# Performance work log

Measured on AMD Instinct MI355X. Metric: run time of the kernel, lower is better.

The kernel has to match this reference:

```python
import jax, jax.numpy as jnp
import numpy as np

DN = ('NCDHW', 'OIDHW', 'NCDHW')

def conv3d(x, w, b=None):
    y = jax.lax.conv_general_dilated(x, w, (1, 1, 1), 'SAME', dimension_numbers=DN)
    if b is not None:
        y = y + b[None, :, None, None, None]
    return y

def adaptive_conv(x, w):
    # x: [N,C,D,H,W], w: [N,27,D,H,W] (L1-normalized over channel dim)
    D, H, W = x.shape[2], x.shape[3], x.shape[4]
    p = jnp.pad(x, ((0, 0), (0, 0), (1, 1), (1, 1), (1, 1)))
    out = jnp.zeros_like(x)
    for i in range(3):
        for j in range(3):
            for k in range(3):
                t = i * 9 + j * 3 + k
                out = out + p[:, :, i:i + D, j:j + H, k:k + W] * w[:, t:t + 1]
    return out

def l1_normalize(w):
    # torch F.normalize(dim=1, p=1): denom clamped to 1e-12
    denom = jnp.maximum(jnp.sum(jnp.abs(w), axis=1, keepdims=True), 1e-12)
    return w / denom

def adaptive_block(x, w1, b1, w2, weights_src=None):
    src = x if weights_src is None else weights_src
    h = jax.nn.relu(conv3d(src, w1, b1))
    w = l1_normalize(conv3d(h, w2))  # [N,27,D,H,W]
    for _ in range(3):
        x = adaptive_conv(x, w)
    return x

def setup_inputs() -> dict:
    key = jax.random.key(0)
    ks = jax.random.split(key, 16)
    s = 0.05
    inp = {
        'x': jax.random.normal(ks[0], (1, 8, 128, 128, 128), dtype=jnp.float32),
        'ac1_w1': jax.random.normal(ks[1], (8, 8, 3, 3, 3), dtype=jnp.float32) * s,
        'ac1_b1': jnp.zeros((8,), dtype=jnp.float32),
        'ac1_w2': jax.random.normal(ks[2], (27, 8, 3, 3, 3), dtype=jnp.float32) * s,
        'ac2_w1': jax.random.normal(ks[3], (8, 8, 3, 3, 3), dtype=jnp.float32) * s,
        'ac2_b1': jnp.zeros((8,), dtype=jnp.float32),
        'ac2_w2': jax.random.normal(ks[4], (27, 8, 3, 3, 3), dtype=jnp.float32) * s,
        'ac3_w1': jax.random.normal(ks[5], (8, 8, 3, 3, 3), dtype=jnp.float32) * s,
        'ac3_b1': jnp.zeros((8,), dtype=jnp.float32),
        'ac3_w2': jax.random.normal(ks[6], (27, 8, 3, 3, 3), dtype=jnp.float32) * s,
        'mid_w': jax.random.normal(ks[7], (8, 8, 3, 3, 3), dtype=jnp.float32) * s,
        'mid_b': jnp.zeros((8,), dtype=jnp.float32),
        'out_w': jax.random.normal(ks[8], (1, 8, 3, 3, 3), dtype=jnp.float32) * s,
        'out_b': jnp.zeros((1,), dtype=jnp.float32),
    }
    return inp

def reference(x, ac1_w1, ac1_b1, ac1_w2, ac2_w1, ac2_b1, ac2_w2,
              ac3_w1, ac3_b1, ac3_w2, mid_w, mid_b, out_w, out_b):
    mid = adaptive_block(x, ac1_w1, ac1_b1, ac1_w2)
    mid = conv3d(mid, mid_w, mid_b)
    mid = adaptive_block(mid, ac2_w1, ac2_b1, ac2_w2)
    final = conv3d(mid, out_w, out_b)  # [N,1,D,H,W]
    final = adaptive_block(final, ac3_w1, ac3_b1, ac3_w2, weights_src=mid)
    return jnp.tanh(final)
```

## Files before the change

### kernel.cpp

```cpp
#include <hip/hip_runtime.h>
#include <math.h>

#define DSZ 128
#define VOX (DSZ*DSZ*DSZ)
#define PD  130

typedef _Float16 half8 __attribute__((ext_vector_type(8)));
typedef _Float16 half4 __attribute__((ext_vector_type(4)));
typedef _Float16 half2v __attribute__((ext_vector_type(2)));
typedef float float4v __attribute__((ext_vector_type(4)));


template<int CH>
__global__ __launch_bounds__(256) void zero_halo(_Float16* __restrict__ P)
{
    const int t = blockIdx.x * 256 + threadIdx.x;
    if (t >= PD * PD) return;
    const int zp = t / PD;
    const int yp = t - zp * PD;
    _Float16* row = P + (size_t)t * PD * CH;
    if (zp == 0 || zp == PD - 1 || yp == 0 || yp == PD - 1) {
        if (CH == 8) {
            half8 zz = {};
            for (int x = 0; x < PD; ++x) *(half8*)&row[x * 8] = zz;
        } else {
            for (int x = 0; x < PD; ++x) row[x] = (_Float16)0.0f;
        }
    } else {
        if (CH == 8) {
            half8 zz = {};
            *(half8*)&row[0] = zz;
            *(half8*)&row[(PD - 1) * 8] = zz;
        } else {
            row[0] = (_Float16)0.0f;
            row[PD - 1] = (_Float16)0.0f;
        }
    }
}

__global__ __launch_bounds__(256) void preformat(const float* __restrict__ w1a, const float* __restrict__ w1b,
                                                 const float* __restrict__ w1c, const float* __restrict__ outw,
                                                 const float* __restrict__ midw,
                                                 const float* __restrict__ w2a, const float* __restrict__ w2b,
                                                 const float* __restrict__ w2c, _Float16* __restrict__ WF)
{
    const int bid = blockIdx.x, tid = threadIdx.x;
    const float* src;
    _Float16* dst;
    int nelem, sz;
    if (bid < 3)       { src = bid == 0 ? w1a : bid == 1 ? w1b : w1c; dst = WF + bid * 3712; nelem = 8 * 216; sz = 16 * 29; }
    else if (bid == 3) { src = outw; dst = WF + 3 * 3712; nelem = 216;     sz = 16 * 29; }
    else if (bid == 4) { src = midw; dst = WF + 4 * 3712; nelem = 8 * 216; sz = 16 * 29; }
    else               { src = bid == 5 ? w2a : bid == 6 ? w2b : w2c; dst = WF + 5 * 3712 + (bid - 5) * 7424; nelem = 27 * 216; sz = 32 * 29; }
    for (int i = tid; i < sz; i += 256) ((half8*)dst)[i] = half8{};
    __syncthreads();
    for (int i = tid; i < nelem; i += 256) {
        const int oc = i / 216;
        const int rem = i - oc * 216;
        const int ic = rem / 27;
        const int tap = rem - ic * 27;
        dst[(oc * 29 + tap) * 8 + ic] = (_Float16)src[i];
    }
}

__global__ __launch_bounds__(256) void cast_hp(const float* __restrict__ in,
                                               _Float16* __restrict__ hp)
{
    const int idx = blockIdx.x * 256 + threadIdx.x;
    const int w = idx & 127;
    const int h = (idx >> 7) & 127;
    const int d = idx >> 14;
    half8 v;
    #pragma unroll
    for (int ic = 0; ic < 8; ++ic) v[ic] = (_Float16)in[(size_t)ic * VOX + idx];
    const int slot = ((d + 1) * PD + (h + 1)) * PD + (w + 1);
    *(half8*)&hp[(size_t)slot * 8] = v;
}

template<bool RELU>
__global__ __launch_bounds__(256) void conv8x8_mfma(const _Float16* __restrict__ DP,
                                                    const _Float16* __restrict__ WF,
                                                    const float* __restrict__ bias,
                                                    _Float16* __restrict__ HO)
{
    __shared__ _Float16 Wr[16 * 29 * 8];
    const int tid = threadIdx.x;
    for (int i = tid; i < 16 * 29; i += 256) ((half8*)Wr)[i] = ((const half8*)WF)[i];
    __syncthreads();

    const int b = ((blockIdx.x & 7) << 10) | (blockIdx.x >> 3);
    const int h0 = (b & 63) << 1;
    const int d  = b >> 6;
    const int lane = tid & 63;
    const int wv   = tid >> 6;
    const int col  = lane & 15;
    const int q    = lane >> 4;

    half8 af[7];
    #pragma unroll
    for (int c = 0; c < 7; ++c)
        af[c] = *(const half8*)&Wr[(col * 29 + (c * 4 + q)) * 8];

    const int base0 = ((d + 1) * PD + (h0 + 1)) * PD + 1 + wv * 32 + col;
    const _Float16* p[7];
    #pragma unroll
    for (int c = 0; c < 7; ++c) {
        const int tap = min(c * 4 + q, 26);
        const int dz = tap / 9, r9 = tap - dz * 9;
        const int dy = r9 / 3,  dx = r9 - dy * 3;
        p[c] = DP + (size_t)(base0 + ((dz - 1) * PD + (dy - 1)) * PD + (dx - 1)) * 8;
    }

    #pragma unroll
    for (int r = 0; r < 2; ++r) {
        #pragma unroll
        for (int t2 = 0; t2 < 2; ++t2) {
            float4v acc = {0.0f, 0.0f, 0.0f, 0.0f};
            #pragma unroll
            for (int c = 0; c < 7; ++c) {
                const half8 bv = *(const half8*)(p[c] + (r * PD + t2 * 16) * 8);
                acc = __builtin_amdgcn_mfma_f32_16x16x32_f16(af[c], bv, acc, 0, 0, 0);
            }
            if (q < 2) {
                const float4v bl = ((const float4v*)bias)[q];
                half4 hv;
                #pragma unroll
                for (int rr = 0; rr < 4; ++rr) {
                    float v = acc[rr] + bl[rr];
                    if (RELU) v = fmaxf(v, 0.0f);
                    hv[rr] = (_Float16)v;
                }
                *(half4*)&HO[(size_t)(base0 + r * PD + t2 * 16) * 8 + q * 4] = hv;
            }
        }
    }
}

__global__ __launch_bounds__(256) void conv8x1_mfma(const _Float16* __restrict__ DP,
                                                    const _Float16* __restrict__ WF,
                                                    const float* __restrict__ bias,
                                                    _Float16* __restrict__ F)
{
    __shared__ _Float16 Wr[16 * 29 * 8];
    const int tid = threadIdx.x;
    for (int i = tid; i < 16 * 29; i += 256) ((half8*)Wr)[i] = ((const half8*)WF)[i];
    __syncthreads();

    const int b = ((blockIdx.x & 7) << 10) | (blockIdx.x >> 3);
    const int h0 = (b & 63) << 1;
    const int d  = b >> 6;
    const int lane = tid & 63;
    const int wv   = tid >> 6;
    const int col  = lane & 15;
    const int q    = lane >> 4;

    half8 af[7];
    #pragma unroll
    for (int c = 0; c < 7; ++c)
        af[c] = *(const half8*)&Wr[(col * 29 + (c * 4 + q)) * 8];

    const int base0 = ((d + 1) * PD + (h0 + 1)) * PD + 1 + wv * 32 + col;
    const _Float16* p[7];
    #pragma unroll
    for (int c = 0; c < 7; ++c) {
        const int tap = min(c * 4 + q, 26);
        const int dz = tap / 9, r9 = tap - dz * 9;
        const int dy = r9 / 3,  dx = r9 - dy * 3;
        p[c] = DP + (size_t)(base0 + ((dz - 1) * PD + (dy - 1)) * PD + (dx - 1)) * 8;
    }

    const float b0 = bias[0];
    #pragma unroll
    for (int r = 0; r < 2; ++r) {
        #pragma unroll
        for (int t2 = 0; t2 < 2; ++t2) {
            float4v acc = {0.0f, 0.0f, 0.0f, 0.0f};
            #pragma unroll
            for (int c = 0; c < 7; ++c) {
                const half8 bv = *(const half8*)(p[c] + (r * PD + t2 * 16) * 8);
                acc = __builtin_amdgcn_mfma_f32_16x16x32_f16(af[c], bv, acc, 0, 0, 0);
            }
            if (q == 0)
                F[base0 + r * PD + t2 * 16] = (_Float16)(acc[0] + b0);
        }
    }
}

__global__ __launch_bounds__(256) void conv8x27n_mfma(const _Float16* __restrict__ HP,
                                                      const _Float16* __restrict__ WF,
                                                      _Float16* __restrict__ WB)
{
    __shared__ _Float16 Wr[32 * 29 * 8];
    const int tid = threadIdx.x;
    for (int i = tid; i < 32 * 29; i += 256) ((half8*)Wr)[i] = ((const half8*)WF)[i];
    __syncthreads();

    const int b = ((blockIdx.x & 7) << 10) | (blockIdx.x >> 3);
    const int h0 = (b & 63) << 1;
    const int d  = b >> 6;
    const int lane = tid & 63;
    const int wv   = tid >> 6;
    const int col  = lane & 15;
    const int q    = lane >> 4;

    half8 af[2][7];
    #pragma unroll
    for (int t = 0; t < 2; ++t)
        #pragma unroll
        for (int c = 0; c < 7; ++c)
            af[t][c] = *(const half8*)&Wr[((t * 16 + col) * 29 + (c * 4 + q)) * 8];

    const int base0 = ((d + 1) * PD + (h0 + 1)) * PD + 1 + wv * 32 + col;
    const _Float16* p[7];
    #pragma unroll
    for (int c = 0; c < 7; ++c) {
        const int tap = min(c * 4 + q, 26);
        const int dz = tap / 9, r9 = tap - dz * 9;
        const int dy = r9 / 3,  dx = r9 - dy * 3;
        p[c] = HP + (size_t)(base0 + ((dz - 1) * PD + (dy - 1)) * PD + (dx - 1)) * 8;
    }

    #pragma unroll
    for (int r = 0; r < 2; ++r) {
        #pragma unroll
        for (int t2 = 0; t2 < 2; ++t2) {
            float4v acc0 = {0.0f, 0.0f, 0.0f, 0.0f};
            float4v acc1 = {0.0f, 0.0f, 0.0f, 0.0f};
            #pragma unroll
            for (int c = 0; c < 7; ++c) {
                const half8 bv = *(const half8*)(p[c] + (r * PD + t2 * 16) * 8);
                acc0 = __builtin_amdgcn_mfma_f32_16x16x32_f16(af[0][c], bv, acc0, 0, 0, 0);
                acc1 = __builtin_amdgcn_mfma_f32_16x16x32_f16(af[1][c], bv, acc1, 0, 0, 0);
            }

            float s = 0.0f;
            #pragma unroll
            for (int rr = 0; rr < 4; ++rr) {
                s += fabsf(acc0[rr]);
                if (16 + q * 4 + rr < 27) s += fabsf(acc1[rr]);
            }
            s += __shfl_xor(s, 16);
            s += __shfl_xor(s, 32);
            const float rcp = 1.0f / fmaxf(s, 1e-12f);

            const int vox = (d << 14) + ((h0 + r) << 7) + wv * 32 + t2 * 16 + col;
            const size_t base = (size_t)vox * 28;
            half4 o0, o1;
            #pragma unroll
            for (int rr = 0; rr < 4; ++rr) {
                o0[rr] = (_Float16)(acc0[rr] * rcp);
                o1[rr] = (_Float16)(acc1[rr] * rcp);
            }
            *(half4*)&WB[base + q * 4] = o0;
            if (q < 3)
                *(half4*)&WB[base + 16 + q * 4] = o1;
        }
    }
}

__global__ __launch_bounds__(256) void aconv8i(const _Float16* __restrict__ in,
                                               const _Float16* __restrict__ wb,
                                               _Float16* __restrict__ out)
{
    __shared__ _Float16 T[12 * 130 * 8];
    const int b = ((blockIdx.x & 7) << 10) | (blockIdx.x >> 3);
    const int h0 = (b & 63) << 1;
    const int d  = b >> 6;
    const int tid = threadIdx.x;

    for (int i = tid; i < 12 * 130; i += 256) {
        const int dz  = i / 520;
        const int rem = i - dz * 520;
        const int yy  = rem / 130;
        const int xs  = rem - yy * 130;
        ((half8*)T)[i] =
            *(const half8*)&in[((size_t)((d + dz) * PD + (h0 + yy)) * PD + xs) * 8];
    }
    __syncthreads();

    const int x   = tid & 127;
    const int ly  = tid >> 7;
    const int idx = b * 256 + tid;

    const size_t wbb = (size_t)idx * 28;
    half4 W[7];
    #pragma unroll
    for (int k = 0; k < 7; ++k) W[k] = *(const half4*)(wb + wbb + k * 4);

    half2v a4[4];
    #pragma unroll
    for (int j = 0; j < 4; ++j) a4[j] = half2v{};

    #pragma unroll
    for (int dz = 0; dz < 3; dz++) {
        #pragma unroll
        for (int dy = 0; dy < 3; dy++) {
            const _Float16* rp = &T[((dz * 4 + (ly + dy)) * 130 + (x + 1)) * 8];
            #pragma unroll
            for (int kw = 0; kw < 3; kw++) {
                const int tap = dz * 9 + dy * 3 + kw;
                const _Float16 wt = W[tap >> 2][tap & 3];
                half2v w2; w2[0] = wt; w2[1] = wt;
                const half8 hv = *(const half8*)(rp + (kw - 1) * 8);
                const half2v* h2 = (const half2v*)&hv;
                #pragma unroll
                for (int j = 0; j < 4; ++j)
                    a4[j] += h2[j] * w2;
            }
        }
    }

    const int s0 = ((d + 1) * PD + (h0 + ly + 1)) * PD + (x + 1);
    half8 o;
    #pragma unroll
    for (int j = 0; j < 4; ++j) { o[2 * j] = a4[j][0]; o[2 * j + 1] = a4[j][1]; }
    *(half8*)&out[(size_t)s0 * 8] = o;
}

template<bool TANH>
__global__ __launch_bounds__(256) void aconv1h(const _Float16* __restrict__ in,
                                               const _Float16* __restrict__ wb,
                                               _Float16* __restrict__ outh,
                                               float* __restrict__ outf)
{
    const int b = ((blockIdx.x & 7) << 10) | (blockIdx.x >> 3);
    const int idx = b * 256 + threadIdx.x;
    const int w = idx & 127;
    const int h = (idx >> 7) & 127;
    const int d = idx >> 14;

    const size_t wbb = (size_t)idx * 28;
    half4 W[7];
    #pragma unroll
    for (int k = 0; k < 7; ++k) W[k] = *(const half4*)(wb + wbb + k * 4);

    const int s0 = ((d + 1) * PD + (h + 1)) * PD + (w + 1);

    float acc = 0.0f;
    #pragma unroll
    for (int dz = 0; dz < 3; dz++) {
        #pragma unroll
        for (int dy = 0; dy < 3; dy++) {
            const _Float16* rp = in + s0 + ((dz - 1) * PD + (dy - 1)) * PD;
            #pragma unroll
            for (int kw = 0; kw < 3; kw++) {
                const int tap = dz * 9 + dy * 3 + kw;
                const _Float16 wt = W[tap >> 2][tap & 3];
                acc = fmaf((float)rp[kw - 1], (float)wt, acc);
            }
        }
    }

    if (TANH) outf[idx] = tanhf(acc);
    else      outh[s0] = (_Float16)acc;
}

extern "C" void kernel_launch(void* const* d_in, const int* in_sizes, int n_in,
                              void* d_out, int out_size, void* d_ws, size_t ws_size,
                              hipStream_t stream)
{
    const float* x      = (const float*)d_in[0];
    const float* ac1_w1 = (const float*)d_in[1];
    const float* ac1_b1 = (const float*)d_in[2];
    const float* ac1_w2 = (const float*)d_in[3];
    const float* ac2_w1 = (const float*)d_in[4];
    const float* ac2_b1 = (const float*)d_in[5];
    const float* ac2_w2 = (const float*)d_in[6];
    const float* ac3_w1 = (const float*)d_in[7];
    const float* ac3_b1 = (const float*)d_in[8];
    const float* ac3_w2 = (const float*)d_in[9];
    const float* mid_w  = (const float*)d_in[10];
    const float* mid_b  = (const float*)d_in[11];
    const float* out_w  = (const float*)d_in[12];
    const float* out_b  = (const float*)d_in[13];
    float* out = (float*)d_out;

    char* ws = (char*)d_ws;
    const size_t PS8 = (size_t)PD * PD * PD * 8 * 2;
    const size_t PS1 = (size_t)PD * PD * PD * 2;
    const size_t WBsz = (size_t)VOX * 28 * 2;
    _Float16* P0 = (_Float16*)(ws);
    _Float16* P1 = (_Float16*)(ws + PS8);
    _Float16* WB = (_Float16*)(ws + 2 * PS8);
    _Float16* F1 = (_Float16*)(ws + 2 * PS8 + WBsz);
    _Float16* G1 = (_Float16*)(ws + 2 * PS8 + WBsz + PS1);
    _Float16* F2 = (_Float16*)(ws + 2 * PS8 + WBsz + 2 * PS1);
    _Float16* WF = (_Float16*)(ws + 2 * PS8 + WBsz + 3 * PS1);
    _Float16* WF8_1  = WF;
    _Float16* WF8_2  = WF + 3712;
    _Float16* WF8_3  = WF + 7424;
    _Float16* WFo    = WF + 11136;
    _Float16* WFmid  = WF + 14848;
    _Float16* WF27_1 = WF + 18560;
    _Float16* WF27_2 = WF + 25984;
    _Float16* WF27_3 = WF + 33408;

    const dim3 blk(256);
    const dim3 gridT(VOX / 256);
    const dim3 gridM(VOX / 256);
    const dim3 gridZ((PD * PD + 255) / 256);

    zero_halo<8><<<gridZ, blk, 0, stream>>>(P0);
    zero_halo<8><<<gridZ, blk, 0, stream>>>(P1);
    zero_halo<1><<<gridZ, blk, 0, stream>>>(F1);
    zero_halo<1><<<gridZ, blk, 0, stream>>>(G1);
    zero_halo<1><<<gridZ, blk, 0, stream>>>(F2);
    preformat<<<dim3(8), blk, 0, stream>>>(ac1_w1, ac2_w1, ac3_w1, out_w, mid_w,
                                           ac1_w2, ac2_w2, ac3_w2, WF);

    cast_hp<<<gridT, blk, 0, stream>>>(x, P0);
    conv8x8_mfma<true ><<<gridM, blk, 0, stream>>>(P0, WF8_1, ac1_b1, P1);
    conv8x27n_mfma<<<gridM, blk, 0, stream>>>(P1, WF27_1, WB);
    aconv8i<<<gridT, blk, 0, stream>>>(P0, WB, P1);
    aconv8i<<<gridT, blk, 0, stream>>>(P1, WB, P0);
    aconv8i<<<gridT, blk, 0, stream>>>(P0, WB, P1);
    conv8x8_mfma<false><<<gridM, blk, 0, stream>>>(P1, WFmid, mid_b, P0);
    conv8x8_mfma<true ><<<gridM, blk, 0, stream>>>(P0, WF8_2, ac2_b1, P1);
    conv8x27n_mfma<<<gridM, blk, 0, stream>>>(P1, WF27_2, WB);
    aconv8i<<<gridT, blk, 0, stream>>>(P0, WB, P1);
    aconv8i<<<gridT, blk, 0, stream>>>(P1, WB, P0);
    aconv8i<<<gridT, blk, 0, stream>>>(P0, WB, P1);
    conv8x8_mfma<true ><<<gridM, blk, 0, stream>>>(P1, WF8_3, ac3_b1, P0);
    conv8x27n_mfma<<<gridM, blk, 0, stream>>>(P0, WF27_3, WB);
    conv8x1_mfma<<<gridM, blk, 0, stream>>>(P1, WFo, out_b, F1);
    aconv1h<false><<<gridT, blk, 0, stream>>>(F1, WB, G1, nullptr);
    aconv1h<false><<<gridT, blk, 0, stream>>>(G1, WB, F2, nullptr);
    aconv1h<true ><<<gridT, blk, 0, stream>>>(F2, WB, nullptr, out);
}
```

Baseline: 749.2 us.

## Process four rows per block in MFMA convs, stage aconv1h tiles in LDS

The conv8x8 and conv8x27 MFMA kernels now cover four output rows per block instead of two, halving the grid and amortising the per-block weight staging and fragment setup. aconv8i issues its per-voxel weight loads before the shared-memory tile fill so the two overlap. aconv1h now stages a 3x4-row input tile in shared memory rather than doing 27 scattered global loads per voxel. The cost is more registers and work per block in the convs and fewer blocks to spread across compute units.

```diff
diff --git a/kernel.cpp b/kernel.cpp
--- a/kernel.cpp
+++ b/kernel.cpp
@@ -88,9 +88,9 @@
     for (int i = tid; i < 16 * 29; i += 256) ((half8*)Wr)[i] = ((const half8*)WF)[i];
     __syncthreads();
 
-    const int b = ((blockIdx.x & 7) << 10) | (blockIdx.x >> 3);
-    const int h0 = (b & 63) << 1;
-    const int d  = b >> 6;
+    const int b = ((blockIdx.x & 7) << 9) | (blockIdx.x >> 3);
+    const int h0 = (b & 31) << 2;
+    const int d  = b >> 5;
     const int lane = tid & 63;
     const int wv   = tid >> 6;
     const int col  = lane & 15;
@@ -112,7 +112,7 @@
     }
 
     #pragma unroll
-    for (int r = 0; r < 2; ++r) {
+    for (int r = 0; r < 4; ++r) {
         #pragma unroll
         for (int t2 = 0; t2 < 2; ++t2) {
             float4v acc = {0.0f, 0.0f, 0.0f, 0.0f};
@@ -195,9 +195,9 @@
     for (int i = tid; i < 32 * 29; i += 256) ((half8*)Wr)[i] = ((const half8*)WF)[i];
     __syncthreads();
 
-    const int b = ((blockIdx.x & 7) << 10) | (blockIdx.x >> 3);
-    const int h0 = (b & 63) << 1;
-    const int d  = b >> 6;
+    const int b = ((blockIdx.x & 7) << 9) | (blockIdx.x >> 3);
+    const int h0 = (b & 31) << 2;
+    const int d  = b >> 5;
     const int lane = tid & 63;
     const int wv   = tid >> 6;
     const int col  = lane & 15;
@@ -221,7 +221,7 @@
     }
 
     #pragma unroll
-    for (int r = 0; r < 2; ++r) {
+    for (int r = 0; r < 4; ++r) {
         #pragma unroll
         for (int t2 = 0; t2 < 2; ++t2) {
             float4v acc0 = {0.0f, 0.0f, 0.0f, 0.0f};
@@ -267,6 +267,12 @@
     const int h0 = (b & 63) << 1;
     const int d  = b >> 6;
     const int tid = threadIdx.x;
+
+    const int idx = b * 256 + tid;
+    const size_t wbb = (size_t)idx * 28;
+    half4 W[7];
+    #pragma unroll
+    for (int k = 0; k < 7; ++k) W[k] = *(const half4*)(wb + wbb + k * 4);
 
     for (int i = tid; i < 12 * 130; i += 256) {
         const int dz  = i / 520;
@@ -278,14 +284,8 @@
     }
     __syncthreads();
 
-    const int x   = tid & 127;
-    const int ly  = tid >> 7;
-    const int idx = b * 256 + tid;
-
-    const size_t wbb = (size_t)idx * 28;
-    half4 W[7];
-    #pragma unroll
-    for (int k = 0; k < 7; ++k) W[k] = *(const half4*)(wb + wbb + k * 4);
+    const int x  = tid & 127;
+    const int ly = tid >> 7;
 
     half2v a4[4];
     #pragma unroll
@@ -323,25 +323,36 @@
                                                _Float16* __restrict__ outh,
                                                float* __restrict__ outf)
 {
+    __shared__ _Float16 T[12 * 130];
     const int b = ((blockIdx.x & 7) << 10) | (blockIdx.x >> 3);
-    const int idx = b * 256 + threadIdx.x;
-    const int w = idx & 127;
-    const int h = (idx >> 7) & 127;
-    const int d = idx >> 14;
-
+    const int h0 = (b & 63) << 1;
+    const int d  = b >> 6;
+    const int tid = threadIdx.x;
+
+    const int idx = b * 256 + tid;
     const size_t wbb = (size_t)idx * 28;
     half4 W[7];
     #pragma unroll
     for (int k = 0; k < 7; ++k) W[k] = *(const half4*)(wb + wbb + k * 4);
 
-    const int s0 = ((d + 1) * PD + (h + 1)) * PD + (w + 1);
+    for (int i = tid; i < 12 * 130; i += 256) {
+        const int dz  = i / 520;
+        const int rem = i - dz * 520;
+        const int yy  = rem / 130;
+        const int xs  = rem - yy * 130;
+        T[i] = in[(size_t)((d + dz) * PD + (h0 + yy)) * PD + xs];
+    }
+    __syncthreads();
+
+    const int x  = tid & 127;
+    const int ly = tid >> 7;
 
     float acc = 0.0f;
     #pragma unroll
     for (int dz = 0; dz < 3; dz++) {
         #pragma unroll
         for (int dy = 0; dy < 3; dy++) {
-            const _Float16* rp = in + s0 + ((dz - 1) * PD + (dy - 1)) * PD;
+            const _Float16* rp = &T[(dz * 4 + (ly + dy)) * 130 + (x + 1)];
             #pragma unroll
             for (int kw = 0; kw < 3; kw++) {
                 const int tap = dz * 9 + dy * 3 + kw;
@@ -351,8 +362,12 @@
         }
     }
 
-    if (TANH) outf[idx] = tanhf(acc);
-    else      outh[s0] = (_Float16)acc;
+    if (TANH) {
+        outf[idx] = tanhf(acc);
+    } else {
+        const int s0 = ((d + 1) * PD + (h0 + ly + 1)) * PD + (x + 1);
+        outh[s0] = (_Float16)acc;
+    }
 }
 
 extern "C" void kernel_launch(void* const* d_in, const int* in_sizes, int n_in,
@@ -397,7 +412,8 @@
 
     const dim3 blk(256);
     const dim3 gridT(VOX / 256);
-    const dim3 gridM(VOX / 256);
+    const dim3 gridM4(VOX / 512);
+    const dim3 gridM2(VOX / 256);
     const dim3 gridZ((PD * PD + 255) / 256);
 
     zero_halo<8><<<gridZ, blk, 0, stream>>>(P0);
@@ -409,20 +425,20 @@
                                            ac1_w2, ac2_w2, ac3_w2, WF);
 
     cast_hp<<<gridT, blk, 0, stream>>>(x, P0);
-    conv8x8_mfma<true ><<<gridM, blk, 0, stream>>>(P0, WF8_1, ac1_b1, P1);
-    conv8x27n_mfma<<<gridM, blk, 0, stream>>>(P1, WF27_1, WB);
+    conv8x8_mfma<true ><<<gridM4, blk, 0, stream>>>(P0, WF8_1, ac1_b1, P1);
+    conv8x27n_mfma<<<gridM4, blk, 0, stream>>>(P1, WF27_1, WB);
     aconv8i<<<gridT, blk, 0, stream>>>(P0, WB, P1);
     aconv8i<<<gridT, blk, 0, stream>>>(P1, WB, P0);
     aconv8i<<<gridT, blk, 0, stream>>>(P0, WB, P1);
-    conv8x8_mfma<false><<<gridM, blk, 0, stream>>>(P1, WFmid, mid_b, P0);
-    conv8x8_mfma<true ><<<gridM, blk, 0, stream>>>(P0, WF8_2, ac2_b1, P1);
-    conv8x27n_mfma<<<gridM, blk, 0, stream>>>(P1, WF27_2, WB);
+    conv8x8_mfma<false><<<gridM4, blk, 0, stream>>>(P1, WFmid, mid_b, P0);
+    conv8x8_mfma<true ><<<gridM4, blk, 0, stream>>>(P0, WF8_2, ac2_b1, P1);
+    conv8x27n_mfma<<<gridM4, blk, 0, stream>>>(P1, WF27_2, WB);
     aconv8i<<<gridT, blk, 0, stream>>>(P0, WB, P1);
     aconv8i<<<gridT, blk, 0, stream>>>(P1, WB, P0);
     aconv8i<<<gridT, blk, 0, stream>>>(P0, WB, P1);
-    conv8x8_mfma<true ><<<gridM, blk, 0, stream>>>(P1, WF8_3, ac3_b1, P0);
-    conv8x27n_mfma<<<gridM, blk, 0, stream>>>(P0, WF27_3, WB);
-    conv8x1_mfma<<<gridM, blk, 0, stream>>>(P1, WFo, out_b, F1);
+    conv8x8_mfma<true ><<<gridM4, blk, 0, stream>>>(P1, WF8_3, ac3_b1, P0);
+    conv8x27n_mfma<<<gridM4, blk, 0, stream>>>(P0, WF27_3, WB);
+    conv8x1_mfma<<<gridM2, blk, 0, stream>>>(P1, WFo, out_b, F1);
     aconv1h<false><<<gridT, blk, 0, stream>>>(F1, WB, G1, nullptr);
     aconv1h<false><<<gridT, blk, 0, stream>>>(G1, WB, F2, nullptr);
     aconv1h<true ><<<gridT, blk, 0, stream>>>(F2, WB, nullptr, out);
```

After: 769.7 us. 2.7% more time.
